# Kernel tuning notes

Measured on AMD Instinct MI355X. Metric: run time of the kernel, lower is better.

The kernel has to match this reference:

```python
import jax, jax.numpy as jnp
import numpy as np

B, L, H, Y = 8, 2500, 512, 8921

def setup_inputs() -> dict:
    key = jax.random.key(0)
    k1, k2, k3, k4, k5 = jax.random.split(key, 5)
    x = jax.random.normal(k1, (B, L, H), dtype=jnp.float32)
    target = (jax.random.uniform(k2, (B, Y), dtype=jnp.float32) < 0.01).astype(jnp.float32)
    # xavier-uniform style scale for [Y, H] linear weights
    lim = float(np.sqrt(6.0 / (Y + H)))
    U_weight = jax.random.uniform(k3, (Y, H), minval=-lim, maxval=lim, dtype=jnp.float32)
    final_weight = jax.random.uniform(k4, (Y, H), minval=-lim, maxval=lim, dtype=jnp.float32)
    final_bias = jax.random.normal(k5, (Y,), dtype=jnp.float32) * 0.01
    return {"x": x, "target": target, "U_weight": U_weight,
            "final_weight": final_weight, "final_bias": final_bias}

def reference(x, target, U_weight, final_weight, final_bias):
    # alpha = softmax over seq of U.weight @ x^T : [B, Y, L]
    scores = jnp.einsum('yh,blh->byl', U_weight, x)
    alpha = jax.nn.softmax(scores, axis=-1)
    # m = alpha @ x : [B, Y, H]
    m = jnp.einsum('byl,blh->byh', alpha, x)
    # y = sum_h final.weight * m + bias : [B, Y]
    y = jnp.einsum('yh,byh->by', final_weight, m) + final_bias
    # BCEWithLogitsLoss (mean reduction), numerically stable
    loss = jnp.mean(jnp.maximum(y, 0.0) - y * target + jnp.log1p(jnp.exp(-jnp.abs(y))))
    return (y, loss)
```

## Files before the change

### kernel.cpp

```cpp
#include <hip/hip_runtime.h>
#include <hip/hip_bf16.h>
#include <cstdint>

#define BDIM 8
#define LDIM 2500
#define HDIM 512
#define YDIM 8921
#define LPAD 2560
#define YPAD 8960
#define NLT 10
#define NYT 70
#define KSTEPS 8

using f32x4  = __attribute__((ext_vector_type(4))) float;
using bf16x8 = __attribute__((ext_vector_type(8))) short;

__device__ __forceinline__ unsigned short f2bf(float f) {
  union { float f; unsigned u; } c; c.f = f;
  unsigned u = c.u;
  unsigned r = (u + 0x7fffu + ((u >> 16) & 1u)) >> 16;
  return (unsigned short)r;
}

__global__ void cvt_x_kernel(const float* __restrict__ x, unsigned short* __restrict__ xb) {
  int e = (blockIdx.x * 256 + threadIdx.x) * 4;
  int b = blockIdx.y;
  int lp = e >> 9;
  int h  = e & 511;
  float4 v = {0.f, 0.f, 0.f, 0.f};
  if (lp < LDIM)
    v = *(const float4*)(x + (((size_t)(b * LDIM + lp)) << 9) + h);
  ushort4 o;
  o.x = f2bf(v.x); o.y = f2bf(v.y); o.z = f2bf(v.z); o.w = f2bf(v.w);
  *(ushort4*)(xb + (((size_t)b * LPAD) << 9) + e) = o;
}

__global__ void cvt_w_kernel(const float* __restrict__ w, unsigned short* __restrict__ wb) {
  int e = (blockIdx.x * 256 + threadIdx.x) * 4;
  int row = e >> 9;
  int col = e & 511;
  float4 v = {0.f, 0.f, 0.f, 0.f};
  if (row < YDIM)
    v = *(const float4*)(w + ((size_t)row << 9) + col);
  ushort4 o;
  o.x = f2bf(v.x); o.y = f2bf(v.y); o.z = f2bf(v.z); o.w = f2bf(v.w);
  *(ushort4*)(wb + e) = o;
}

__global__ __launch_bounds__(512, 2) void fused_kernel(
    const unsigned short* __restrict__ xb,
    const unsigned short* __restrict__ ub,
    const unsigned short* __restrict__ fb,
    float* __restrict__ part) {
  __shared__ __align__(16) unsigned char smem[131072];

  const int wid = blockIdx.x;
  const int b   = wid & 7;
  const int q   = wid >> 3;
  const int yt  = q / NLT;
  const int lt  = q - yt * NLT;
  const int tid = threadIdx.x;
  const int lane = tid & 63;
  const int wave = tid >> 6;
  const int wm = wave >> 2;
  const int wn = wave & 3;
  const int r16  = lane & 15;
  const int kgrp = lane >> 4;
  const int kg16 = kgrp << 4;
  const int xorR = (r16 & 7) << 4;

  const int srow = tid >> 3;
  const int slot = tid & 7;
  const unsigned short* asrc[4];
#pragma unroll
  for (int i = 0; i < 4; ++i) {
    int m = i * 64 + srow;
    const unsigned short* Wsrc = (m & 16) ? fb : ub;
    int yrow = yt * 128 + ((m >> 5) << 4) + (m & 15);
    asrc[i] = Wsrc + ((size_t)yrow << 9) + ((slot ^ (m & 7)) << 3);
  }
  const unsigned short* bsrc[4];
#pragma unroll
  for (int i = 0; i < 4; ++i) {
    int r = i * 64 + srow;
    int lrow = lt * 256 + r;
    bsrc[i] = xb + (((size_t)(b * LPAD + lrow)) << 9) + ((slot ^ (r & 7)) << 3);
  }
  const int ldst = tid * 16;

#pragma unroll
  for (int i = 0; i < 4; ++i) {
    __builtin_amdgcn_global_load_lds(
        (const __attribute__((address_space(1))) void*)(asrc[i]),
        (__attribute__((address_space(3))) void*)(smem + i * 8192 + ldst), 16, 0, 0);
    __builtin_amdgcn_global_load_lds(
        (const __attribute__((address_space(1))) void*)(bsrc[i]),
        (__attribute__((address_space(3))) void*)(smem + 32768 + i * 8192 + ldst), 16, 0, 0);
  }
  __syncthreads();

  f32x4 acc[8][4];
#pragma unroll
  for (int mt = 0; mt < 8; ++mt)
#pragma unroll
    for (int nt = 0; nt < 4; ++nt) acc[mt][nt] = {0.f, 0.f, 0.f, 0.f};

  for (int ks = 0; ks < KSTEPS; ++ks) {
    const int cur = ks & 1;
    if (ks < KSTEPS - 1) {
      const int ko = (ks + 1) << 6;
      unsigned char* Ad = smem + (cur ^ 1) * 65536;
#pragma unroll
      for (int i = 0; i < 4; ++i) {
        __builtin_amdgcn_global_load_lds(
            (const __attribute__((address_space(1))) void*)(asrc[i] + ko),
            (__attribute__((address_space(3))) void*)(Ad + i * 8192 + ldst), 16, 0, 0);
        __builtin_amdgcn_global_load_lds(
            (const __attribute__((address_space(1))) void*)(bsrc[i] + ko),
            (__attribute__((address_space(3))) void*)(Ad + 32768 + i * 8192 + ldst), 16, 0, 0);
      }
    }

    const unsigned char* Ab = smem + cur * 65536;
    const unsigned char* Bb = Ab + 32768;
#pragma unroll
    for (int kk = 0; kk < 2; ++kk) {
      const int ko = ((kk << 6) + kg16) ^ xorR;
      bf16x8 bfr[4];
#pragma unroll
      for (int nt = 0; nt < 4; ++nt)
        bfr[nt] = *(const bf16x8*)(Bb + (wn * 64 + nt * 16 + r16) * 128 + ko);
#pragma unroll
      for (int mt = 0; mt < 8; ++mt) {
        bf16x8 af = *(const bf16x8*)(Ab + (wm * 128 + mt * 16 + r16) * 128 + ko);
#pragma unroll
        for (int nt = 0; nt < 4; ++nt)
          acc[mt][nt] = __builtin_amdgcn_mfma_f32_16x16x32_bf16(af, bfr[nt], acc[mt][nt], 0, 0, 0);
      }
    }
    __syncthreads();
  }

  const bool tail = (lt == NLT - 1);
  float* comb = (float*)smem;
#pragma unroll
  for (int p = 0; p < 4; ++p) {
#pragma unroll
    for (int r = 0; r < 4; ++r) {
      float mt_l = fmaxf(fmaxf(acc[2 * p][0][r], acc[2 * p][1][r]),
                         fmaxf(acc[2 * p][2][r], acc[2 * p][3][r]));
      mt_l = fmaxf(mt_l, __shfl_xor(mt_l, 1));
      mt_l = fmaxf(mt_l, __shfl_xor(mt_l, 2));
      mt_l = fmaxf(mt_l, __shfl_xor(mt_l, 4));
      mt_l = fmaxf(mt_l, __shfl_xor(mt_l, 8));
      float e_ = 0.f, o_ = 0.f;
#pragma unroll
      for (int nt = 0; nt < 4; ++nt) {
        float s = acc[2 * p][nt][r];
        float t = acc[2 * p + 1][nt][r];
        float pv = __expf(s - mt_l);
        if (tail) {
          int lg = lt * 256 + wn * 64 + nt * 16 + r16;
          if (lg >= LDIM) pv = 0.f;
        }
        e_ += pv;
        o_ += pv * t;
      }
      e_ += __shfl_xor(e_, 1); o_ += __shfl_xor(o_, 1);
      e_ += __shfl_xor(e_, 2); o_ += __shfl_xor(o_, 2);
      e_ += __shfl_xor(e_, 4); o_ += __shfl_xor(o_, 4);
      e_ += __shfl_xor(e_, 8); o_ += __shfl_xor(o_, 8);
      if (r16 == 0) {
        int y_loc = (wm * 4 + p) * 16 + kgrp * 4 + r;
        float* c = comb + (y_loc * 4 + wn) * 3;
        c[0] = mt_l; c[1] = e_; c[2] = o_;
      }
    }
  }
  __syncthreads();
  if (tid < 128) {
    float* c = comb + tid * 12;
    float M = fmaxf(fmaxf(c[0], c[3]), fmaxf(c[6], c[9]));
    float E = 0.f, O = 0.f;
#pragma unroll
    for (int w = 0; w < 4; ++w) {
      float sw = __expf(c[w * 3] - M);
      E += sw * c[w * 3 + 1];
      O += sw * c[w * 3 + 2];
    }
    size_t gy = (size_t)(b * NYT + yt) * 128 + tid;
    float* pp = part + (gy * NLT + lt) * 3;
    pp[0] = M; pp[1] = E; pp[2] = O;
  }
}

__global__ void combine_kernel(const float* __restrict__ part,
                               const float* __restrict__ bias,
                               float* __restrict__ out) {
  int g = blockIdx.x * 256 + threadIdx.x;
  if (g >= BDIM * NYT * 128) return;
  const float* pp = part + (size_t)g * (NLT * 3);
  float M = -1e30f;
#pragma unroll
  for (int i = 0; i < NLT; ++i) M = fmaxf(M, pp[i * 3]);
  float E = 0.f, O = 0.f;
#pragma unroll
  for (int i = 0; i < NLT; ++i) {
    float w = __expf(pp[i * 3] - M);
    E += w * pp[i * 3 + 1];
    O += w * pp[i * 3 + 2];
  }
  int y128 = g & 127;
  int rest = g >> 7;
  int yt = rest % NYT;
  int b  = rest / NYT;
  int y = yt * 128 + y128;
  if (y < YDIM)
    out[b * YDIM + y] = O / E + bias[y];
}

__global__ void loss_part(const float* __restrict__ yv, const float* __restrict__ tgt,
                          float* __restrict__ partl) {
  __shared__ float red[256];
  int tid = threadIdx.x;
  int base = blockIdx.x * 1024;
  float s = 0.f;
#pragma unroll
  for (int j = 0; j < 4; ++j) {
    int i = base + j * 256 + tid;
    if (i < BDIM * YDIM) {
      float y = yv[i];
      float t = tgt[i];
      s += fmaxf(y, 0.f) - y * t + log1pf(expf(-fabsf(y)));
    }
  }
  red[tid] = s;
  __syncthreads();
  for (int off = 128; off > 0; off >>= 1) {
    if (tid < off) red[tid] += red[tid + off];
    __syncthreads();
  }
  if (tid == 0) partl[blockIdx.x] = red[0];
}

__global__ void loss_final(const float* __restrict__ partl, float* __restrict__ out) {
  __shared__ float red[128];
  int tid = threadIdx.x;
  red[tid] = (tid < 70) ? partl[tid] : 0.f;
  __syncthreads();
  for (int off = 64; off > 0; off >>= 1) {
    if (tid < off) red[tid] += red[tid + off];
    __syncthreads();
  }
  if (tid == 0) out[BDIM * YDIM] = red[0] / (float)(BDIM * YDIM);
}

extern "C" void kernel_launch(void* const* d_in, const int* in_sizes, int n_in,
                              void* d_out, int out_size, void* d_ws, size_t ws_size,
                              hipStream_t stream) {
  const float* x    = (const float*)d_in[0];
  const float* tgt  = (const float*)d_in[1];
  const float* U    = (const float*)d_in[2];
  const float* F    = (const float*)d_in[3];
  const float* bias = (const float*)d_in[4];
  float* out = (float*)d_out;

  unsigned short* xb = (unsigned short*)d_ws;
  unsigned short* ub = xb + (size_t)BDIM * LPAD * HDIM;
  unsigned short* fw = ub + (size_t)YPAD * HDIM;
  float* partf = (float*)(fw + (size_t)YPAD * HDIM);
  float* partl = partf + (size_t)BDIM * NYT * 128 * NLT * 3;

  cvt_x_kernel<<<dim3(1280, BDIM), 256, 0, stream>>>(x, xb);
  cvt_w_kernel<<<4480, 256, 0, stream>>>(U, ub);
  cvt_w_kernel<<<4480, 256, 0, stream>>>(F, fw);
  fused_kernel<<<BDIM * NYT * NLT, 512, 0, stream>>>(xb, ub, fw, partf);
  combine_kernel<<<(BDIM * NYT * 128 + 255) / 256, 256, 0, stream>>>(partf, bias, out);
  loss_part<<<70, 256, 0, stream>>>(out, tgt, partl);
  loss_final<<<1, 128, 0, stream>>>(partl, out);
}
```

Baseline: 530.2 us.

## Repartition waves to own full L span and interleave loads with MFMA phases

Each wave now owns 16 output Y rows (U and final pairs) across the full 256-wide L tile, instead of a 2x4 wave grid. This removes the cross-wave shared-memory softmax combine and its extra barrier, and lets the partial results be written straight from registers. The K-step is split into four quarter phases, each with its own fine-grained vmcnt/lgkmcnt waits, barriers and s_setprio, with the global-to-LDS prefetch loads spread across those phases. The trade-off is more B-fragment LDS reads per wave, because every wave now reads the whole B tile, plus many more barriers per step.

New measurement: 492.8 us. 7.1% less time.

```diff
diff --git a/kernel.cpp b/kernel.cpp
--- a/kernel.cpp
+++ b/kernel.cpp
@@ -47,6 +47,46 @@
   *(ushort4*)(wb + e) = o;
 }
 
+#define BAR() __builtin_amdgcn_s_barrier()
+#define LGKM0()                                                     \
+  do {                                                              \
+    asm volatile("s_waitcnt lgkmcnt(0)" ::: "memory");              \
+    __builtin_amdgcn_sched_barrier(0);                              \
+  } while (0)
+#define VMW(N)                                                      \
+  do {                                                              \
+    asm volatile("s_waitcnt vmcnt(" #N ")" ::: "memory");           \
+    __builtin_amdgcn_sched_barrier(0);                              \
+  } while (0)
+#define GLD(SD, SRC, DOF)                                           \
+  __builtin_amdgcn_global_load_lds(                                 \
+      (const __attribute__((address_space(1))) void*)(SRC),         \
+      (__attribute__((address_space(3))) void*)((SD) + (DOF)), 16, 0, 0)
+
+#define RDB(P)                                                      \
+  do {                                                              \
+    _Pragma("unroll")                                               \
+    for (int j = 0; j < 4; ++j) {                                   \
+      const unsigned char* _r = Bb + ((P) * 64 + j * 16 + r16) * 128; \
+      bfr[j][0] = *(const bf16x8*)(_r + koB0);                      \
+      bfr[j][1] = *(const bf16x8*)(_r + koB1);                      \
+    }                                                               \
+  } while (0)
+
+#define MFMAQ(P)                                                    \
+  do {                                                              \
+    _Pragma("unroll")                                               \
+    for (int kk = 0; kk < 2; ++kk) {                                \
+      _Pragma("unroll")                                             \
+      for (int j = 0; j < 4; ++j) {                                 \
+        acc[0][(P) * 4 + j] = __builtin_amdgcn_mfma_f32_16x16x32_bf16( \
+            afr[0][kk], bfr[j][kk], acc[0][(P) * 4 + j], 0, 0, 0);  \
+        acc[1][(P) * 4 + j] = __builtin_amdgcn_mfma_f32_16x16x32_bf16( \
+            afr[1][kk], bfr[j][kk], acc[1][(P) * 4 + j], 0, 0, 0);  \
+      }                                                             \
+    }                                                               \
+  } while (0)
+
 __global__ __launch_bounds__(512, 2) void fused_kernel(
     const unsigned short* __restrict__ xb,
     const unsigned short* __restrict__ ub,
@@ -61,136 +101,128 @@
   const int lt  = q - yt * NLT;
   const int tid = threadIdx.x;
   const int lane = tid & 63;
-  const int wave = tid >> 6;
-  const int wm = wave >> 2;
-  const int wn = wave & 3;
+  const int w    = tid >> 6;
   const int r16  = lane & 15;
   const int kgrp = lane >> 4;
   const int kg16 = kgrp << 4;
   const int xorR = (r16 & 7) << 4;
-
-  const int srow = tid >> 3;
-  const int slot = tid & 7;
-  const unsigned short* asrc[4];
+  const int koB0 = kg16 ^ xorR;
+  const int koB1 = (64 + kg16) ^ xorR;
+  const int w32  = w * 32;
+  const int lane16 = lane * 16;
+  const int colofs = ((lane & 7) ^ (lane >> 3)) << 3;
+
+  const unsigned short* asp[4]; int adst[4];
 #pragma unroll
   for (int i = 0; i < 4; ++i) {
-    int m = i * 64 + srow;
+    int m = w32 + i * 8 + (lane >> 3);
     const unsigned short* Wsrc = (m & 16) ? fb : ub;
     int yrow = yt * 128 + ((m >> 5) << 4) + (m & 15);
-    asrc[i] = Wsrc + ((size_t)yrow << 9) + ((slot ^ (m & 7)) << 3);
-  }
-  const unsigned short* bsrc[4];
-#pragma unroll
-  for (int i = 0; i < 4; ++i) {
-    int r = i * 64 + srow;
-    int lrow = lt * 256 + r;
-    bsrc[i] = xb + (((size_t)(b * LPAD + lrow)) << 9) + ((slot ^ (r & 7)) << 3);
-  }
-  const int ldst = tid * 16;
-
-#pragma unroll
-  for (int i = 0; i < 4; ++i) {
-    __builtin_amdgcn_global_load_lds(
-        (const __attribute__((address_space(1))) void*)(asrc[i]),
-        (__attribute__((address_space(3))) void*)(smem + i * 8192 + ldst), 16, 0, 0);
-    __builtin_amdgcn_global_load_lds(
-        (const __attribute__((address_space(1))) void*)(bsrc[i]),
-        (__attribute__((address_space(3))) void*)(smem + 32768 + i * 8192 + ldst), 16, 0, 0);
-  }
-  __syncthreads();
-
-  f32x4 acc[8][4];
-#pragma unroll
-  for (int mt = 0; mt < 8; ++mt)
-#pragma unroll
-    for (int nt = 0; nt < 4; ++nt) acc[mt][nt] = {0.f, 0.f, 0.f, 0.f};
+    asp[i]  = Wsrc + ((size_t)yrow << 9) + colofs;
+    adst[i] = w32 * 128 + i * 1024 + lane16;
+  }
+  const unsigned short* bp[4]; int bdst[4];
+#pragma unroll
+  for (int i = 0; i < 2; ++i) {
+    int lr0 = w * 16 + i * 8 + (lane >> 3);
+    bp[i]      = xb + (((size_t)(b * LPAD + lt * 256 + lr0)) << 9) + colofs;
+    bdst[i]    = 32768 + (w * 16 + i * 8) * 128 + lane16;
+    int lr1 = 128 + w * 16 + i * 8 + (lane >> 3);
+    bp[2 + i]  = xb + (((size_t)(b * LPAD + lt * 256 + lr1)) << 9) + colofs;
+    bdst[2 + i] = 32768 + (128 + w * 16 + i * 8) * 128 + lane16;
+  }
+
+  {
+    unsigned char* sd = (unsigned char*)smem;
+    GLD(sd, bp[0], bdst[0]); GLD(sd, bp[1], bdst[1]);
+#pragma unroll
+    for (int i = 0; i < 4; ++i) GLD(sd, asp[i], adst[i]);
+    GLD(sd, bp[2], bdst[2]); GLD(sd, bp[3], bdst[3]);
+  }
+  VMW(2);
+  BAR();
+
+  f32x4 acc[2][16];
+#pragma unroll
+  for (int mt = 0; mt < 2; ++mt)
+#pragma unroll
+    for (int nt = 0; nt < 16; ++nt) acc[mt][nt] = {0.f, 0.f, 0.f, 0.f};
 
   for (int ks = 0; ks < KSTEPS; ++ks) {
-    const int cur = ks & 1;
-    if (ks < KSTEPS - 1) {
-      const int ko = (ks + 1) << 6;
-      unsigned char* Ad = smem + (cur ^ 1) * 65536;
-#pragma unroll
-      for (int i = 0; i < 4; ++i) {
-        __builtin_amdgcn_global_load_lds(
-            (const __attribute__((address_space(1))) void*)(asrc[i] + ko),
-            (__attribute__((address_space(3))) void*)(Ad + i * 8192 + ldst), 16, 0, 0);
-        __builtin_amdgcn_global_load_lds(
-            (const __attribute__((address_space(1))) void*)(bsrc[i] + ko),
-            (__attribute__((address_space(3))) void*)(Ad + 32768 + i * 8192 + ldst), 16, 0, 0);
+    const unsigned char* Ab = (const unsigned char*)smem + ((ks & 1) << 16);
+    const unsigned char* Bb = Ab + 32768;
+    unsigned char* sd = (unsigned char*)smem + (((ks & 1) ^ 1) << 16);
+    const int ko = (ks + 1) << 6;
+    const bool st = (ks < KSTEPS - 1);
+    bf16x8 afr[2][2];
+    bf16x8 bfr[4][2];
+
+    RDB(0);
+#pragma unroll
+    for (int mt = 0; mt < 2; ++mt) {
+      const unsigned char* _a = Ab + (w32 + mt * 16 + r16) * 128;
+      afr[mt][0] = *(const bf16x8*)(_a + koB0);
+      afr[mt][1] = *(const bf16x8*)(_a + koB1);
+    }
+    if (st) { GLD(sd, bp[0] + ko, bdst[0]); GLD(sd, bp[1] + ko, bdst[1]); }
+    BAR(); LGKM0();
+    __builtin_amdgcn_s_setprio(1); MFMAQ(0); __builtin_amdgcn_s_setprio(0);
+    BAR();
+
+    RDB(1);
+    if (st) { GLD(sd, asp[0] + ko, adst[0]); GLD(sd, asp[1] + ko, adst[1]); }
+    BAR(); LGKM0();
+    __builtin_amdgcn_s_setprio(1); MFMAQ(1); __builtin_amdgcn_s_setprio(0);
+    if (st) { VMW(4); } else { VMW(0); }
+    BAR();
+
+    RDB(2);
+    if (st) { GLD(sd, asp[2] + ko, adst[2]); GLD(sd, asp[3] + ko, adst[3]); }
+    BAR(); LGKM0();
+    __builtin_amdgcn_s_setprio(1); MFMAQ(2); __builtin_amdgcn_s_setprio(0);
+    BAR();
+
+    RDB(3);
+    if (st) { GLD(sd, bp[2] + ko, bdst[2]); GLD(sd, bp[3] + ko, bdst[3]); }
+    BAR(); LGKM0();
+    __builtin_amdgcn_s_setprio(1); MFMAQ(3); __builtin_amdgcn_s_setprio(0);
+    VMW(2);
+    BAR();
+  }
+
+  const bool tail = (lt == NLT - 1);
+#pragma unroll
+  for (int r = 0; r < 4; ++r) {
+    float mv = -1e30f;
+#pragma unroll
+    for (int nt = 0; nt < 16; ++nt) mv = fmaxf(mv, acc[0][nt][r]);
+    mv = fmaxf(mv, __shfl_xor(mv, 1));
+    mv = fmaxf(mv, __shfl_xor(mv, 2));
+    mv = fmaxf(mv, __shfl_xor(mv, 4));
+    mv = fmaxf(mv, __shfl_xor(mv, 8));
+    float e_ = 0.f, o_ = 0.f;
+#pragma unroll
+    for (int nt = 0; nt < 16; ++nt) {
+      float s = acc[0][nt][r];
+      float t = acc[1][nt][r];
+      float pv = __expf(s - mv);
+      if (tail) {
+        int lg = lt * 256 + nt * 16 + r16;
+        if (lg >= LDIM) pv = 0.f;
       }
+      e_ += pv;
+      o_ += pv * t;
     }
-
-    const unsigned char* Ab = smem + cur * 65536;
-    const unsigned char* Bb = Ab + 32768;
-#pragma unroll
-    for (int kk = 0; kk < 2; ++kk) {
-      const int ko = ((kk << 6) + kg16) ^ xorR;
-      bf16x8 bfr[4];
-#pragma unroll
-      for (int nt = 0; nt < 4; ++nt)
-        bfr[nt] = *(const bf16x8*)(Bb + (wn * 64 + nt * 16 + r16) * 128 + ko);
-#pragma unroll
-      for (int mt = 0; mt < 8; ++mt) {
-        bf16x8 af = *(const bf16x8*)(Ab + (wm * 128 + mt * 16 + r16) * 128 + ko);
-#pragma unroll
-        for (int nt = 0; nt < 4; ++nt)
-          acc[mt][nt] = __builtin_amdgcn_mfma_f32_16x16x32_bf16(af, bfr[nt], acc[mt][nt], 0, 0, 0);
-      }
+    e_ += __shfl_xor(e_, 1); o_ += __shfl_xor(o_, 1);
+    e_ += __shfl_xor(e_, 2); o_ += __shfl_xor(o_, 2);
+    e_ += __shfl_xor(e_, 4); o_ += __shfl_xor(o_, 4);
+    e_ += __shfl_xor(e_, 8); o_ += __shfl_xor(o_, 8);
+    if (r16 == 0) {
+      int y_loc = w * 16 + kgrp * 4 + r;
+      size_t gy = (size_t)(b * NYT + yt) * 128 + y_loc;
+      float* pp = part + (gy * NLT + lt) * 3;
+      pp[0] = mv; pp[1] = e_; pp[2] = o_;
     }
-    __syncthreads();
-  }
-
-  const bool tail = (lt == NLT - 1);
-  float* comb = (float*)smem;
-#pragma unroll
-  for (int p = 0; p < 4; ++p) {
-#pragma unroll
-    for (int r = 0; r < 4; ++r) {
-      float mt_l = fmaxf(fmaxf(acc[2 * p][0][r], acc[2 * p][1][r]),
-                         fmaxf(acc[2 * p][2][r], acc[2 * p][3][r]));
-      mt_l = fmaxf(mt_l, __shfl_xor(mt_l, 1));
-      mt_l = fmaxf(mt_l, __shfl_xor(mt_l, 2));
-      mt_l = fmaxf(mt_l, __shfl_xor(mt_l, 4));
-      mt_l = fmaxf(mt_l, __shfl_xor(mt_l, 8));
-      float e_ = 0.f, o_ = 0.f;
-#pragma unroll
-      for (int nt = 0; nt < 4; ++nt) {
-        float s = acc[2 * p][nt][r];
-        float t = acc[2 * p + 1][nt][r];
-        float pv = __expf(s - mt_l);
-        if (tail) {
-          int lg = lt * 256 + wn * 64 + nt * 16 + r16;
-          if (lg >= LDIM) pv = 0.f;
-        }
-        e_ += pv;
-        o_ += pv * t;
-      }
-      e_ += __shfl_xor(e_, 1); o_ += __shfl_xor(o_, 1);
-      e_ += __shfl_xor(e_, 2); o_ += __shfl_xor(o_, 2);
-      e_ += __shfl_xor(e_, 4); o_ += __shfl_xor(o_, 4);
-      e_ += __shfl_xor(e_, 8); o_ += __shfl_xor(o_, 8);
-      if (r16 == 0) {
-        int y_loc = (wm * 4 + p) * 16 + kgrp * 4 + r;
-        float* c = comb + (y_loc * 4 + wn) * 3;
-        c[0] = mt_l; c[1] = e_; c[2] = o_;
-      }
-    }
-  }
-  __syncthreads();
-  if (tid < 128) {
-    float* c = comb + tid * 12;
-    float M = fmaxf(fmaxf(c[0], c[3]), fmaxf(c[6], c[9]));
-    float E = 0.f, O = 0.f;
-#pragma unroll
-    for (int w = 0; w < 4; ++w) {
-      float sw = __expf(c[w * 3] - M);
-      E += sw * c[w * 3 + 1];
-      O += sw * c[w * 3 + 2];
-    }
-    size_t gy = (size_t)(b * NYT + yt) * 128 + tid;
-    float* pp = part + (gy * NLT + lt) * 3;
-    pp[0] = M; pp[1] = E; pp[2] = O;
   }
 }
 
```
